# Kernel optimization log

Hardware: AMD Instinct MI355X
Metric: run time of the kernel (lower is better)

The kernel has to match this reference:

```python
import jax, jax.numpy as jnp
import numpy as np

B, T, C, H = 4, 1024, 1024, 16
D = C // H
SINK = 4
EPS_LN = 1e-5

def _layernorm(x, w, b):
    mu = jnp.mean(x, axis=-1, keepdims=True)
    var = jnp.mean(jnp.square(x - mu), axis=-1, keepdims=True)
    return (x - mu) * jax.lax.rsqrt(var + EPS_LN) * w + b

def setup_inputs() -> dict:
    key = jax.random.key(0)
    ks = jax.random.split(key, 8)
    s = 0.02
    inp = {
        "x": jax.random.normal(ks[0], (B, T, C), jnp.float32),
        "attention_mask": jnp.ones((B, T), jnp.int32),
        "W_attn": jax.random.normal(ks[1], (C, 3 * C), jnp.float32) * s,
        "b_attn": jnp.zeros((3 * C,), jnp.float32),
        "W_proj": jax.random.normal(ks[2], (C, C), jnp.float32) * s,
        "b_proj": jnp.zeros((C,), jnp.float32),
        "ln1_w": jnp.ones((C,), jnp.float32),
        "ln1_b": jnp.zeros((C,), jnp.float32),
        "ln2_w": jnp.ones((C,), jnp.float32),
        "ln2_b": jnp.zeros((C,), jnp.float32),
        "W_fc": jax.random.normal(ks[3], (C, 4 * C), jnp.float32) * s,
        "b_fc": jnp.zeros((4 * C,), jnp.float32),
        "W_fc2": jax.random.normal(ks[4], (4 * C, C), jnp.float32) * s,
        "b_fc2": jnp.zeros((C,), jnp.float32),
        "threshold": jnp.float32((0 + 1) / 12 * 0.01),  # layer_idx=0, n_layer=12, final_token_threshold=0.01
    }
    return inp

def reference(x, attention_mask, W_attn, b_attn, W_proj, b_proj,
              ln1_w, ln1_b, ln2_w, ln2_b, W_fc, b_fc, W_fc2, b_fc2, threshold):
    # --- attention on ln_1(x), with explicit weight materialization ---
    h = _layernorm(x, ln1_w, ln1_b)
    qkv = h @ W_attn + b_attn                       # (B,T,3C)
    q, k, v = jnp.split(qkv, 3, axis=-1)
    q = q.reshape(B, T, H, D).transpose(0, 2, 1, 3)  # (B,H,T,D)
    k = k.reshape(B, T, H, D).transpose(0, 2, 1, 3)
    v = v.reshape(B, T, H, D).transpose(0, 2, 1, 3)
    scores = jnp.einsum("bhqd,bhkd->bhqk", q, k) * (1.0 / np.sqrt(D))
    causal = jnp.tril(jnp.ones((T, T), bool))[None, None]          # (1,1,T,T)
    keep = causal & (attention_mask[:, None, None, :] != 0)        # (B,1,T,T)
    scores = jnp.where(keep, scores, -jnp.inf)
    att = jax.nn.softmax(scores, axis=-1)
    att = jnp.nan_to_num(att, nan=0.0)              # fully-masked rows -> 0
    y = jnp.einsum("bhqk,bhkd->bhqd", att, v)       # (B,H,T,D)
    y = y.transpose(0, 2, 1, 3).reshape(B, T, C)
    y = y @ W_proj + b_proj                         # dropout=0.0 -> identity

    # --- cumulative-attention importance ---
    imp = att.sum(axis=2).mean(axis=1)              # (B,T): attention received
    pos_norm = jnp.arange(T, 0, -1, dtype=jnp.float32) / T
    imp = imp / (pos_norm[None, :] + 1e-8)
    imp = imp.at[:, :SINK].set(imp.max() + 1.0)

    # --- residual + MLP ---
    x2 = x + y
    m = _layernorm(x2, ln2_w, ln2_b)
    mlp = jax.nn.gelu(m @ W_fc + b_fc, approximate=False) @ W_fc2 + b_fc2
    out = x2 + mlp

    # --- hard pruning mask ---
    mask = (imp >= threshold).astype(jnp.float32)
    mask = mask.at[:, :SINK].set(1.0)
    mask = mask * attention_mask.astype(jnp.float32)
    return out, mask, imp
```

## Files before the change

### kernel.cpp

```cpp
#include <hip/hip_runtime.h>
#include <math.h>

constexpr int Bc = 4, Tc = 1024, Cc = 1024, Hc = 16, Dc = 64, SINKc = 4;
constexpr float EPS_LN = 1e-5f;

typedef __bf16 bf16x4 __attribute__((ext_vector_type(4)));
typedef __bf16 bf16x8 __attribute__((ext_vector_type(8)));
typedef float  f32x4  __attribute__((ext_vector_type(4)));

__global__ __launch_bounds__(256) void transpose_bf16(
    const float* __restrict__ W, __bf16* __restrict__ Wt, int K, int N)
{
    __shared__ float S[32][33];
    int n0 = blockIdx.x * 32, k0 = blockIdx.y * 32;
    int t = threadIdx.x;
    int r = t >> 3, c4 = (t & 7) * 4;
    float4 v = *(const float4*)(W + (size_t)(k0 + r) * N + n0 + c4);
    S[r][c4+0] = v.x; S[r][c4+1] = v.y; S[r][c4+2] = v.z; S[r][c4+3] = v.w;
    __syncthreads();
    bf16x4 o = { (__bf16)S[c4+0][r], (__bf16)S[c4+1][r],
                 (__bf16)S[c4+2][r], (__bf16)S[c4+3][r] };
    *(bf16x4*)(Wt + (size_t)(n0 + r) * K + k0 + c4) = o;
}

__global__ __launch_bounds__(256) void ln_kernel(
    const float* __restrict__ x, const float* __restrict__ w,
    const float* __restrict__ bsh, __bf16* __restrict__ outp)
{
    int row = blockIdx.x;
    const float* xr = x + (size_t)row * Cc;
    int tid = threadIdx.x;

    float4 xl = reinterpret_cast<const float4*>(xr)[tid];
    float s  = xl.x + xl.y + xl.z + xl.w;
    float s2 = xl.x*xl.x + xl.y*xl.y + xl.z*xl.z + xl.w*xl.w;
    for (int off = 32; off; off >>= 1) {
        s  += __shfl_down(s,  off, 64);
        s2 += __shfl_down(s2, off, 64);
    }
    __shared__ float r1[4], r2[4];
    if ((tid & 63) == 0) { r1[tid >> 6] = s; r2[tid >> 6] = s2; }
    __syncthreads();
    float mu  = (r1[0]+r1[1]+r1[2]+r1[3]) * (1.0f / Cc);
    float var = (r2[0]+r2[1]+r2[2]+r2[3]) * (1.0f / Cc) - mu*mu;
    float rstd = rsqrtf(var + EPS_LN);

    float4 wl = reinterpret_cast<const float4*>(w)[tid];
    float4 bl = reinterpret_cast<const float4*>(bsh)[tid];
    bf16x4 o = { (__bf16)((xl.x - mu) * rstd * wl.x + bl.x),
                 (__bf16)((xl.y - mu) * rstd * wl.y + bl.y),
                 (__bf16)((xl.z - mu) * rstd * wl.z + bl.z),
                 (__bf16)((xl.w - mu) * rstd * wl.w + bl.w) };
    *(bf16x4*)(outp + (size_t)row * Cc + tid * 4) = o;
}

template <int EPI, typename OutT, int TM, int OCC, int MAP>
__global__ __launch_bounds__(256, OCC) void gemm_bf16(
    const __bf16* __restrict__ A, const __bf16* __restrict__ Bt,
    const float* __restrict__ bias, const float* R,
    OutT* Cm, int M, int N, int K)
{
    __shared__ __bf16 As[2][TM * 32];
    __shared__ __bf16 Bs[2][128 * 32];

    const int tid  = threadIdx.x;
    const int wave = tid >> 6, lane = tid & 63;
    const int wm = wave >> 1, wn = wave & 1;
    const int lr = lane & 15, lc = lane >> 4;

    const int nblk = gridDim.x;
    const int per = nblk >> 3;
    const int rank = (blockIdx.x & 7) * per + (blockIdx.x >> 3);
    int bx, by;
    if (MAP == 0) {
        const int gx = N >> 7;
        const int GM = 8;
        const int grp = rank / (GM * gx);
        const int rem = rank % (GM * gx);
        by = grp * GM + (rem % GM);
        bx = rem / GM;
    } else {
        const int gy = M / TM;
        bx = rank / gy;
        by = rank % gy;
    }

    f32x4 acc[TM / 32][4] = {};

    const int srow = lane >> 2;
    const int cphys = lane & 3;

    for (int k0 = 0; k0 < K; k0 += 64) {
        __syncthreads();
        #pragma unroll
        for (int ii = wave; ii < (TM / 16) * 2; ii += 4) {
            int idx = ii >> 1, c = ii & 1;
            int rloc = idx * 16 + srow;
            int clog = (cphys - (rloc >> 1)) & 3;
            const __bf16* ga = A + (size_t)(by * TM + rloc) * K + k0 + c * 32 + clog * 8;
            __builtin_amdgcn_global_load_lds(
                (const __attribute__((address_space(1))) void*)ga,
                (__attribute__((address_space(3))) void*)(&As[c][idx * 512]), 16, 0, 0);
        }
        #pragma unroll
        for (int ii = wave; ii < 16; ii += 4) {
            int idx = ii >> 1, c = ii & 1;
            int rloc = idx * 16 + srow;
            int clog = (cphys - (rloc >> 1)) & 3;
            const __bf16* gb = Bt + (size_t)(bx * 128 + rloc) * K + k0 + c * 32 + clog * 8;
            __builtin_amdgcn_global_load_lds(
                (const __attribute__((address_space(1))) void*)gb,
                (__attribute__((address_space(3))) void*)(&Bs[c][idx * 512]), 16, 0, 0);
        }
        __syncthreads();

        #pragma unroll
        for (int s = 0; s < 2; s++) {
            bf16x8 af[TM / 32], bfr[4];
            #pragma unroll
            for (int i = 0; i < TM / 32; i++) {
                int ra = wm * (TM / 2) + i * 16 + lr;
                int ca = (lc + (ra >> 1)) & 3;
                af[i] = *(const bf16x8*)(&As[s][ra * 32 + ca * 8]);
            }
            #pragma unroll
            for (int j = 0; j < 4; j++) {
                int rb = wn * 64 + j * 16 + lr;
                int cb = (lc + (rb >> 1)) & 3;
                bfr[j] = *(const bf16x8*)(&Bs[s][rb * 32 + cb * 8]);
            }
            #pragma unroll
            for (int i = 0; i < TM / 32; i++)
                #pragma unroll
                for (int j = 0; j < 4; j++)
                    acc[i][j] = __builtin_amdgcn_mfma_f32_16x16x32_bf16(
                        af[i], bfr[j], acc[i][j], 0, 0, 0);
        }
    }

    #pragma unroll
    for (int j = 0; j < 4; j++) {
        int n = bx * 128 + wn * 64 + j * 16 + lr;
        float bv = bias[n];
        #pragma unroll
        for (int i = 0; i < TM / 32; i++) {
            int m0 = by * TM + wm * (TM / 2) + i * 16 + lc * 4;
            #pragma unroll
            for (int e = 0; e < 4; e++) {
                float t = acc[i][j][e] + bv;
                if (EPI == 1) t = 0.5f * t * (1.0f + erff(t * 0.70710678118654752f));
                if (EPI == 2) t += R[(size_t)(m0 + e) * N + n];
                Cm[(size_t)(m0 + e) * N + n] = (OutT)t;
            }
        }
    }
}

__global__ __launch_bounds__(256, 3) void attn_mfma(
    const __bf16* __restrict__ qkv, const int* __restrict__ amask,
    __bf16* __restrict__ ybuf, float* __restrict__ lbuf)
{
    __shared__ __bf16 Kb[2][64 * 32];
    __shared__ __align__(16) __bf16 Vt[64][72];
    __shared__ __align__(16) __bf16 Ps[64][72];

    int blk = blockIdx.x;
    int idx = blk & 15, h = (blk >> 4) & 15, b = blk >> 8;
    int idx2 = (idx + h + b) & 15;
    int p2 = idx2 >> 1;
    int qt = (idx2 & 1) ? p2 : (15 - p2);
    int q0 = qt * 64;

    int tid = threadIdx.x, wave = tid >> 6, lane = tid & 63;
    int quad = lane >> 4, l15 = lane & 15;
    const int srow = lane >> 2, cphys = lane & 3;
    const size_t RS = 3 * Cc;
    const size_t bT = (size_t)b * Tc;

    bf16x8 qf[2];
    {
        const __bf16* qrow = qkv + (bT + q0 + wave * 16 + l15) * RS + h * 64 + quad * 8;
        qf[0] = *(const bf16x8*)qrow;
        qf[1] = *(const bf16x8*)(qrow + 32);
    }

    float l_part[4] = {0.f, 0.f, 0.f, 0.f};
    f32x4 Oacc[4] = {};

    for (int kt = 0; kt <= qt; kt++) {
        int k0 = kt * 64;
        __syncthreads();

        #pragma unroll
        for (int c = 0; c < 2; c++) {
            int rloc = wave * 16 + srow;
            int clog = (cphys - (rloc >> 1)) & 3;
            const __bf16* g = qkv + (bT + k0 + rloc) * RS + Cc + h * 64 + c * 32 + clog * 8;
            __builtin_amdgcn_global_load_lds(
                (const __attribute__((address_space(1))) void*)g,
                (__attribute__((address_space(3))) void*)(&Kb[c][wave * 512]), 16, 0, 0);
        }
        {
            int kk = lane, dbase = wave * 16;
            const __bf16* vrow = qkv + (bT + k0 + kk) * RS + 2 * Cc + h * 64 + dbase;
            bf16x8 v0 = *(const bf16x8*)vrow;
            bf16x8 v1 = *(const bf16x8*)(vrow + 8);
            #pragma unroll
            for (int j = 0; j < 8; j++) Vt[dbase + j][kk] = v0[j];
            #pragma unroll
            for (int j = 0; j < 8; j++) Vt[dbase + 8 + j][kk] = v1[j];
        }
        int am4[4];
        #pragma unroll
        for (int j = 0; j < 4; j++) am4[j] = amask[bT + k0 + j * 16 + l15];
        __syncthreads();

        f32x4 Sacc[4] = {};
        #pragma unroll
        for (int c = 0; c < 2; c++)
            #pragma unroll
            for (int j = 0; j < 4; j++) {
                int rb = j * 16 + l15;
                int cb = (quad + (rb >> 1)) & 3;
                bf16x8 kf = *(const bf16x8*)(&Kb[c][rb * 32 + cb * 8]);
                Sacc[j] = __builtin_amdgcn_mfma_f32_16x16x32_bf16(qf[c], kf, Sacc[j], 0, 0, 0);
            }

        #pragma unroll
        for (int e = 0; e < 4; e++) {
            int qg = q0 + wave * 16 + quad * 4 + e;
            #pragma unroll
            for (int j = 0; j < 4; j++) {
                int kg = k0 + j * 16 + l15;
                float p = (kg <= qg && am4[j] != 0)
                              ? __expf(Sacc[j][e] * 0.125f) : 0.f;
                l_part[e] += p;
                Ps[wave * 16 + quad * 4 + e][j * 16 + l15] = (__bf16)p;
            }
        }
        __syncthreads();

        #pragma unroll
        for (int c2 = 0; c2 < 2; c2++) {
            bf16x8 pa = *(const bf16x8*)(&Ps[wave * 16 + l15][quad * 8 + c2 * 32]);
            #pragma unroll
            for (int j2 = 0; j2 < 4; j2++) {
                bf16x8 vb = *(const bf16x8*)(&Vt[j2 * 16 + l15][quad * 8 + c2 * 32]);
                Oacc[j2] = __builtin_amdgcn_mfma_f32_16x16x32_bf16(pa, vb, Oacc[j2], 0, 0, 0);
            }
        }
    }

    #pragma unroll
    for (int e = 0; e < 4; e++) {
        float l = l_part[e];
        #pragma unroll
        for (int off = 8; off; off >>= 1) l += __shfl_xor(l, off, 64);
        int qg = q0 + wave * 16 + quad * 4 + e;
        float invl = (l > 0.f) ? 1.f / l : 0.f;
        #pragma unroll
        for (int j2 = 0; j2 < 4; j2++)
            ybuf[(bT + qg) * Cc + h * 64 + j2 * 16 + l15] = (__bf16)(Oacc[j2][e] * invl);
        if (l15 == 0)
            lbuf[(size_t)(b * Hc + h) * Tc + qg] = l;
    }
}

__global__ __launch_bounds__(256, 4) void imp_mfma(
    const __bf16* __restrict__ qkv, const int* __restrict__ amask,
    const float* __restrict__ lbuf, float* __restrict__ impbuf)
{
    __shared__ __bf16 Qb[2][64 * 32];
    __shared__ float rls[64];

    int blk = blockIdx.x;
    int idx = blk & 15, h = (blk >> 4) & 15, b = blk >> 8;
    int idx2 = (idx + h + b) & 15;
    int p2 = idx2 >> 1;
    int kt = (idx2 & 1) ? (15 - p2) : p2;
    int k0 = kt * 64;

    int tid = threadIdx.x, wave = tid >> 6, lane = tid & 63;
    int quad = lane >> 4, l15 = lane & 15;
    const int srow = lane >> 2, cphys = lane & 3;
    const size_t RS = 3 * Cc;
    const size_t bT = (size_t)b * Tc;
    const size_t mlrow = (size_t)(b * Hc + h) * Tc;

    bf16x8 kf[2];
    {
        const __bf16* krow = qkv + (bT + k0 + wave * 16 + l15) * RS + Cc + h * 64 + quad * 8;
        kf[0] = *(const bf16x8*)krow;
        kf[1] = *(const bf16x8*)(krow + 32);
    }
    int amk[4];
    #pragma unroll
    for (int e = 0; e < 4; e++) amk[e] = amask[bT + k0 + wave * 16 + quad * 4 + e];

    float sums[4] = {0.f, 0.f, 0.f, 0.f};

    for (int qt = kt; qt < 16; qt++) {
        int q0 = qt * 64;
        __syncthreads();
        #pragma unroll
        for (int c = 0; c < 2; c++) {
            int rloc = wave * 16 + srow;
            int clog = (cphys - (rloc >> 1)) & 3;
            const __bf16* g = qkv + (bT + q0 + rloc) * RS + h * 64 + c * 32 + clog * 8;
            __builtin_amdgcn_global_load_lds(
                (const __attribute__((address_space(1))) void*)g,
                (__attribute__((address_space(3))) void*)(&Qb[c][wave * 512]), 16, 0, 0);
        }
        if (tid < 64) {
            float l = lbuf[mlrow + q0 + tid];
            rls[tid] = (l > 0.f) ? 1.f / l : 0.f;
        }
        __syncthreads();

        f32x4 Sacc[4] = {};
        #pragma unroll
        for (int c = 0; c < 2; c++)
            #pragma unroll
            for (int j = 0; j < 4; j++) {
                int rb = j * 16 + l15;
                int cb = (quad + (rb >> 1)) & 3;
                bf16x8 qb = *(const bf16x8*)(&Qb[c][rb * 32 + cb * 8]);
                Sacc[j] = __builtin_amdgcn_mfma_f32_16x16x32_bf16(kf[c], qb, Sacc[j], 0, 0, 0);
            }

        #pragma unroll
        for (int j = 0; j < 4; j++) {
            int qg = q0 + j * 16 + l15;
            float rl = rls[j * 16 + l15];
            #pragma unroll
            for (int e = 0; e < 4; e++) {
                int kg = k0 + wave * 16 + quad * 4 + e;
                if (kg <= qg && amk[e] != 0 && rl > 0.f)
                    sums[e] += __expf(Sacc[j][e] * 0.125f) * rl;
            }
        }
    }

    #pragma unroll
    for (int e = 0; e < 4; e++) {
        float s = sums[e];
        #pragma unroll
        for (int off = 8; off; off >>= 1) s += __shfl_xor(s, off, 64);
        if (l15 == 0)
            atomicAdd(&impbuf[bT + k0 + wave * 16 + quad * 4 + e], s);
    }
}

__global__ __launch_bounds__(1024) void finalize_kernel(
    const float* __restrict__ impbuf, const int* __restrict__ amask,
    const float* __restrict__ thr, float* __restrict__ out_mask,
    float* __restrict__ out_imp)
{
    __shared__ float red[16];
    int tid = threadIdx.x;
    float vloc[4];
    float gmax = -INFINITY;
    #pragma unroll
    for (int it = 0; it < 4; it++) {
        int i = tid + it * 1024;
        int tt = i % Tc;
        float posn = (float)(Tc - tt) / (float)Tc;
        float v = impbuf[i] * (1.0f / Hc) / (posn + 1e-8f);
        vloc[it] = v;
        gmax = fmaxf(gmax, v);
    }
    for (int off = 32; off; off >>= 1) gmax = fmaxf(gmax, __shfl_down(gmax, off, 64));
    if ((tid & 63) == 0) red[tid >> 6] = gmax;
    __syncthreads();
    float gm = red[0];
    #pragma unroll
    for (int i = 1; i < 16; i++) gm = fmaxf(gm, red[i]);

    float t = thr[0];
    #pragma unroll
    for (int it = 0; it < 4; it++) {
        int i = tid + it * 1024;
        int tt = i % Tc;
        float v = vloc[it];
        if (tt < SINKc) v = gm + 1.0f;
        float mk = (v >= t) ? 1.f : 0.f;
        if (tt < SINKc) mk = 1.f;
        mk *= (float)amask[i];
        out_imp[i]  = v;
        out_mask[i] = mk;
    }
}

extern "C" void kernel_launch(void* const* d_in, const int* in_sizes, int n_in,
                              void* d_out, int out_size, void* d_ws, size_t ws_size,
                              hipStream_t stream)
{
    const float* x      = (const float*)d_in[0];
    const int*   amask  = (const int*)  d_in[1];
    const float* W_attn = (const float*)d_in[2];
    const float* b_attn = (const float*)d_in[3];
    const float* W_proj = (const float*)d_in[4];
    const float* b_proj = (const float*)d_in[5];
    const float* ln1w   = (const float*)d_in[6];
    const float* ln1b   = (const float*)d_in[7];
    const float* ln2w   = (const float*)d_in[8];
    const float* ln2b   = (const float*)d_in[9];
    const float* W_fc   = (const float*)d_in[10];
    const float* b_fc   = (const float*)d_in[11];
    const float* W_fc2  = (const float*)d_in[12];
    const float* b_fc2  = (const float*)d_in[13];
    const float* thr    = (const float*)d_in[14];

    float* out      = (float*)d_out;
    float* out_mask = out + (size_t)Bc * Tc * Cc;
    float* out_imp  = out_mask + (size_t)Bc * Tc;

    char* wsb = (char*)d_ws;
    __bf16* qkvbf = (__bf16*)wsb;
    __bf16* hbf   = (__bf16*)(wsb + 25165824);
    __bf16* ybf   = (__bf16*)(wsb + 33554432);
    __bf16* fcbf  = (__bf16*)(wsb + 41943040);
    __bf16* WaT   = (__bf16*)(wsb + 75497472);
    __bf16* WpT   = (__bf16*)(wsb + 81788928);
    __bf16* WfT   = (__bf16*)(wsb + 83886080);
    __bf16* Wf2T  = (__bf16*)(wsb + 92274688);
    float*  lbuf  = (float*)(wsb + 100663296);
    float*  impb  = (float*)(wsb + 100925440);

    const int M = Bc * Tc;

    transpose_bf16<<<dim3(3*Cc/32, Cc/32), 256, 0, stream>>>(W_attn, WaT, Cc, 3*Cc);
    transpose_bf16<<<dim3(Cc/32,   Cc/32), 256, 0, stream>>>(W_proj, WpT, Cc, Cc);
    transpose_bf16<<<dim3(4*Cc/32, Cc/32), 256, 0, stream>>>(W_fc,   WfT, Cc, 4*Cc);
    transpose_bf16<<<dim3(Cc/32, 4*Cc/32), 256, 0, stream>>>(W_fc2,  Wf2T, 4*Cc, Cc);

    ln_kernel<<<M, 256, 0, stream>>>(x, ln1w, ln1b, hbf);
    gemm_bf16<0, __bf16, 128, 2, 0><<<(3*Cc/128) * (M/128), 256, 0, stream>>>(
        hbf, WaT, b_attn, nullptr, qkvbf, M, 3*Cc, Cc);
    hipMemsetAsync(impb, 0, (size_t)Bc * Tc * sizeof(float), stream);
    attn_mfma<<<Bc * Hc * 16, 256, 0, stream>>>(qkvbf, amask, ybf, lbuf);
    gemm_bf16<2, float, 64, 3, 1><<<(Cc/128) * (M/64), 256, 0, stream>>>(
        ybf, WpT, b_proj, x, out, M, Cc, Cc);
    imp_mfma<<<Bc * Hc * 16, 256, 0, stream>>>(qkvbf, amask, lbuf, impb);
    ln_kernel<<<M, 256, 0, stream>>>(out, ln2w, ln2b, hbf);
    gemm_bf16<1, __bf16, 128, 2, 0><<<(4*Cc/128) * (M/128), 256, 0, stream>>>(
        hbf, WfT, b_fc, nullptr, fcbf, M, 4*Cc, Cc);
    gemm_bf16<2, float, 64, 3, 1><<<(Cc/128) * (M/64), 256, 0, stream>>>(
        fcbf, Wf2T, b_fc2, out, out, M, Cc, 4*Cc);
    finalize_kernel<<<1, 1024, 0, stream>>>(impb, amask, thr, out_mask, out_imp);
}
```

Baseline: 375.0 us.

## Add direct global-to-LDS GEMM with swizzled layout and grouped tile ordering

Adds a new GEMM kernel for the QKV and FC1 projections. It loads A and B tiles straight into shared memory with global_load_lds, using an XOR-style swizzled column layout to avoid bank conflicts, and steps K by 64 per barrier pair. Blocks are remapped in groups of eight row tiles across the interleaved block index to improve L2 reuse. The loop is single-buffered with two barriers per step, so there is no overlap of loads with MFMA work, and the lane-to-address mapping of the direct LDS load must match the read swizzle.

Result: no change. 369.1 us (-1.6%).

```diff
diff --git a/kernel.cpp b/kernel.cpp
--- a/kernel.cpp
+++ b/kernel.cpp
@@ -52,6 +52,101 @@
                  (__bf16)((xl.z - mu) * rstd * wl.z + bl.z),
                  (__bf16)((xl.w - mu) * rstd * wl.w + bl.w) };
     *(bf16x4*)(outp + (size_t)row * Cc + tid * 4) = o;
+}
+
+template <int EPI, typename OutT, int TM>
+__global__ __launch_bounds__(256, 2) void gemm_r0(
+    const __bf16* __restrict__ A, const __bf16* __restrict__ Bt,
+    const float* __restrict__ bias, const float* R,
+    OutT* Cm, int M, int N, int K)
+{
+    __shared__ __bf16 As[2][TM * 32];
+    __shared__ __bf16 Bs[2][128 * 32];
+
+    const int tid  = threadIdx.x;
+    const int wave = tid >> 6, lane = tid & 63;
+    const int wm = wave >> 1, wn = wave & 1;
+    const int lr = lane & 15, lc = lane >> 4;
+
+    const int gx = N >> 7;
+    const int nblk = gridDim.x;
+    const int per = nblk >> 3;
+    const int rank = (blockIdx.x & 7) * per + (blockIdx.x >> 3);
+    const int GM = 8;
+    const int grp = rank / (GM * gx);
+    const int rem = rank % (GM * gx);
+    const int by = grp * GM + (rem % GM);
+    const int bx = rem / GM;
+
+    f32x4 acc[TM / 32][4] = {};
+
+    const int srow = lane >> 2;
+    const int cphys = lane & 3;
+
+    for (int k0 = 0; k0 < K; k0 += 64) {
+        __syncthreads();
+        #pragma unroll
+        for (int ii = wave; ii < (TM / 16) * 2; ii += 4) {
+            int idx = ii >> 1, c = ii & 1;
+            int rloc = idx * 16 + srow;
+            int clog = (cphys - (rloc >> 1)) & 3;
+            const __bf16* ga = A + (size_t)(by * TM + rloc) * K + k0 + c * 32 + clog * 8;
+            __builtin_amdgcn_global_load_lds(
+                (const __attribute__((address_space(1))) void*)ga,
+                (__attribute__((address_space(3))) void*)(&As[c][idx * 512]), 16, 0, 0);
+        }
+        #pragma unroll
+        for (int ii = wave; ii < 16; ii += 4) {
+            int idx = ii >> 1, c = ii & 1;
+            int rloc = idx * 16 + srow;
+            int clog = (cphys - (rloc >> 1)) & 3;
+            const __bf16* gb = Bt + (size_t)(bx * 128 + rloc) * K + k0 + c * 32 + clog * 8;
+            __builtin_amdgcn_global_load_lds(
+                (const __attribute__((address_space(1))) void*)gb,
+                (__attribute__((address_space(3))) void*)(&Bs[c][idx * 512]), 16, 0, 0);
+        }
+        __syncthreads();
+
+        #pragma unroll
+        for (int s = 0; s < 2; s++) {
+            bf16x8 af[TM / 32], bfr[4];
+            #pragma unroll
+            for (int i = 0; i < TM / 32; i++) {
+                int ra = wm * (TM / 2) + i * 16 + lr;
+                int ca = (lc + (ra >> 1)) & 3;
+                af[i] = *(const bf16x8*)(&As[s][ra * 32 + ca * 8]);
+            }
+            #pragma unroll
+            for (int j = 0; j < 4; j++) {
+                int rb = wn * 64 + j * 16 + lr;
+                int cb = (lc + (rb >> 1)) & 3;
+                bfr[j] = *(const bf16x8*)(&Bs[s][rb * 32 + cb * 8]);
+            }
+            #pragma unroll
+            for (int i = 0; i < TM / 32; i++)
+                #pragma unroll
+                for (int j = 0; j < 4; j++)
+                    acc[i][j] = __builtin_amdgcn_mfma_f32_16x16x32_bf16(
+                        af[i], bfr[j], acc[i][j], 0, 0, 0);
+        }
+    }
+
+    #pragma unroll
+    for (int j = 0; j < 4; j++) {
+        int n = bx * 128 + wn * 64 + j * 16 + lr;
+        float bv = bias[n];
+        #pragma unroll
+        for (int i = 0; i < TM / 32; i++) {
+            int m0 = by * TM + wm * (TM / 2) + i * 16 + lc * 4;
+            #pragma unroll
+            for (int e = 0; e < 4; e++) {
+                float t = acc[i][j][e] + bv;
+                if (EPI == 1) t = 0.5f * t * (1.0f + erff(t * 0.70710678118654752f));
+                if (EPI == 2) t += R[(size_t)(m0 + e) * N + n];
+                Cm[(size_t)(m0 + e) * N + n] = (OutT)t;
+            }
+        }
+    }
 }
 
 template <int EPI, typename OutT, int TM, int OCC, int MAP>
@@ -435,7 +530,7 @@
     transpose_bf16<<<dim3(Cc/32, 4*Cc/32), 256, 0, stream>>>(W_fc2,  Wf2T, 4*Cc, Cc);
 
     ln_kernel<<<M, 256, 0, stream>>>(x, ln1w, ln1b, hbf);
-    gemm_bf16<0, __bf16, 128, 2, 0><<<(3*Cc/128) * (M/128), 256, 0, stream>>>(
+    gemm_r0<0, __bf16, 128><<<(3*Cc/128) * (M/128), 256, 0, stream>>>(
         hbf, WaT, b_attn, nullptr, qkvbf, M, 3*Cc, Cc);
     hipMemsetAsync(impb, 0, (size_t)Bc * Tc * sizeof(float), stream);
     attn_mfma<<<Bc * Hc * 16, 256, 0, stream>>>(qkvbf, amask, ybf, lbuf);
@@ -443,7 +538,7 @@
         ybf, WpT, b_proj, x, out, M, Cc, Cc);
     imp_mfma<<<Bc * Hc * 16, 256, 0, stream>>>(qkvbf, amask, lbuf, impb);
     ln_kernel<<<M, 256, 0, stream>>>(out, ln2w, ln2b, hbf);
-    gemm_bf16<1, __bf16, 128, 2, 0><<<(4*Cc/128) * (M/128), 256, 0, stream>>>(
+    gemm_r0<1, __bf16, 128><<<(4*Cc/128) * (M/128), 256, 0, stream>>>(
         hbf, WfT, b_fc, nullptr, fcbf, M, 4*Cc, Cc);
     gemm_bf16<2, float, 64, 3, 1><<<(Cc/128) * (M/64), 256, 0, stream>>>(
         fcbf, Wf2T, b_fc2, out, out, M, Cc, 4*Cc);
```
